# Kernel tuning notes

Hardware: AMD Instinct MI355X
Metric: run time of the kernel (lower is better)

The kernel has to match this reference:

```python
import jax, jax.numpy as jnp
import numpy as np

B, LAT, NF, IMG, N_CALLS = 8, 512, 64, 128, 4
N_LAYERS = int(np.ceil(np.log2(IMG) - np.log2(16))) + 1  # 4 resolutions: 16,32,64,128
CF = 3  # SinSobel perception factor: identity + sobel_x + sobel_y
FIN, FH, FOUT = NF * CF, NF, NF * 2  # gated => 2*n_filter out of dyna block
P_SIZES = [FH * FIN, FH, FOUT * FH, FOUT, FOUT * FIN, FOUT]
P_OFFS = np.cumsum([0] + P_SIZES)
P_TOT = int(P_OFFS[-1])

_g1 = np.exp(-0.5 * np.array([-1.0, 0.0, 1.0]) ** 2)
_gk = np.outer(_g1, _g1); _gk = _gk / _gk.sum()
GAUSS_K = jnp.asarray(_gk, jnp.float32)
SOBEL_X = jnp.asarray(np.array([[-1, 0, 1], [-2, 0, 2], [-1, 0, 1]], np.float32) / 8.0)
SOBEL_Y = SOBEL_X.T


def _dwconv3(x, k):
    # depthwise 3x3 conv, 'same' padding; x: [B,C,H,W], k: [3,3]
    C = x.shape[1]
    kern = jnp.broadcast_to(k[None, None], (C, 1, 3, 3)).astype(x.dtype)
    return jax.lax.conv_general_dilated(
        x, kern, (1, 1), ((1, 1), (1, 1)),
        dimension_numbers=('NCHW', 'OIHW', 'NCHW'), feature_group_count=C)


def sin_sobel(x):
    # perception: [x, sobel_x(x), sobel_y(x)] -> 3*C channels
    return jnp.concatenate([x, _dwconv3(x, SOBEL_X), _dwconv3(x, SOBEL_Y)], axis=1)


def inst_norm(x, eps=1e-5):
    m = x.mean((2, 3), keepdims=True)
    v = x.var((2, 3), keepdims=True)
    return (x - m) * jax.lax.rsqrt(v + eps)


def up2_blur(x, gk):
    b, c, h, w = x.shape
    x = jax.image.resize(x, (b, c, 2 * h, 2 * w), 'bilinear')  # align_corners=False
    return _dwconv3(x, gk)


def dyna_block(x, lat, hyper_w, hyper_b):
    # hypernetwork generates per-sample 1x1-conv residual block weights
    p = lat @ hyper_w + hyper_b  # [B, P_TOT]
    w1 = p[:, P_OFFS[0]:P_OFFS[1]].reshape(-1, FH, FIN)
    b1 = p[:, P_OFFS[1]:P_OFFS[2]]
    w2 = p[:, P_OFFS[2]:P_OFFS[3]].reshape(-1, FOUT, FH)
    b2 = p[:, P_OFFS[3]:P_OFFS[4]]
    ws = p[:, P_OFFS[4]:P_OFFS[5]].reshape(-1, FOUT, FIN)
    bs = p[:, P_OFFS[5]:P_OFFS[6]]
    h = jax.nn.relu(jnp.einsum('bihw,boi->bohw', x, w1) + b1[:, :, None, None])
    y = jnp.einsum('bihw,boi->bohw', h, w2) + b2[:, :, None, None]
    s = jnp.einsum('bihw,boi->bohw', x, ws) + bs[:, :, None, None]
    return s + y


def setup_inputs() -> dict:
    key = jax.random.key(0)
    ks = jax.random.split(key, 8)
    return dict(
        lat=jax.random.normal(ks[0], (B, LAT), jnp.float32),
        ca_noise=jax.random.normal(ks[1], (B, NF, 16, 16), jnp.float32),
        seed=jax.random.normal(ks[2], (1, NF, 1, 1), jnp.float32),  # spatially constant seed
        leak_factor=jnp.asarray(0.1, jnp.float32),
        hyper_w=jax.random.normal(ks[3], (LAT, P_TOT), jnp.float32) * 0.02,
        hyper_b=jnp.zeros((P_TOT,), jnp.float32),
        res1_w=jax.random.normal(ks[4], (NF, NF), jnp.float32) / np.sqrt(NF).astype(np.float32),
        res1_b=jnp.zeros((NF,), jnp.float32),
        res2_w=jax.random.normal(ks[5], (NF, NF), jnp.float32) / np.sqrt(NF).astype(np.float32),
        res2_b=jnp.zeros((NF,), jnp.float32),
        outc_w=jax.random.normal(ks[6], (3, NF), jnp.float32) / np.sqrt(NF).astype(np.float32),
        outc_b=jnp.zeros((3,), jnp.float32),
    )


def reference(lat, ca_noise, seed, leak_factor, hyper_w, hyper_b,
              res1_w, res1_b, res2_w, res2_b, outc_w, outc_b):
    # seed init branch: constant seed -> instance_norm -> 0, plus blurred ca_noise
    out = inst_norm(jnp.broadcast_to(seed, (B, NF, 16, 16)))
    out = out + _dwconv3(ca_noise, GAUSS_K)  # in_ds (resize 16->16 is identity)
    lf = jnp.clip(leak_factor, 0.001, 1000.0)
    for c in range(N_LAYERS * N_CALLS):
        z = sin_sobel(out)
        z = inst_norm(z)
        z = dyna_block(z, lat, hyper_w, hyper_b)
        z, g = jnp.split(z, 2, axis=1)  # gated
        z = z * jax.nn.sigmoid(g)
        out = out + lf * z
        if c < N_LAYERS * N_CALLS - 1 and c % N_CALLS == N_CALLS - 1:
            out = up2_blur(out, GAUSS_K)
    # out_conv: resize to IMG is identity here; 1x1 residual block + 1x1 conv
    h = jax.nn.relu(jnp.einsum('bihw,oi->bohw', out, res1_w) + res1_b[None, :, None, None])
    r = jnp.einsum('bihw,oi->bohw', h, res2_w) + res2_b[None, :, None, None]
    y = jnp.einsum('bihw,oi->bohw', out + r, outc_w) + outc_b[None, :, None, None]
    out_raw = y
    return jnp.clip(y, -1.0, 1.0), out_raw
```

## Files before the change

### kernel.cpp

```cpp
#include <hip/hip_runtime.h>
#include <math.h>

#define B 8
#define LATD 512
#define PT 45376
#define FIN 192
#define FH 64
#define OW1 0
#define OB1 12288
#define OW2 12352
#define OB2 20544
#define OWS 20672
#define OBS 45248
#define KC 16

__device__ __forceinline__ float gk_at(int ky, int kx){
  const float a = 0.60653065971263342f;
  const float inv = 1.0f / ((1.0f + 2.0f*a) * (1.0f + 2.0f*a));
  float wy = (ky==1) ? 1.0f : a;
  float wx = (kx==1) ? 1.0f : a;
  return wy * wx * inv;
}

__global__ void k_hyper(const float* __restrict__ lat, const float* __restrict__ hw,
                        const float* __restrict__ hb, float* __restrict__ p){
  __shared__ float slat[B*LATD];
  for (int idx = threadIdx.x; idx < B*LATD; idx += 256) slat[idx] = lat[idx];
  __syncthreads();
  int j = blockIdx.x*256 + threadIdx.x;
  if (j >= PT) return;
  float acc[B];
#pragma unroll
  for (int b=0;b<B;++b) acc[b]=0.f;
  for (int k=0;k<LATD;++k){
    float w = hw[(size_t)k*PT + j];
#pragma unroll
    for (int b=0;b<B;++b) acc[b] = fmaf(slat[b*LATD+k], w, acc[b]);
  }
  float bias = hb[j];
#pragma unroll
  for (int b=0;b<B;++b) p[(size_t)b*PT + j] = acc[b] + bias;
}

__global__ void k_init(const float* __restrict__ noise, float* __restrict__ out){
  int bc = blockIdx.x;
  int t = threadIdx.x;
  int y = t >> 4, x = t & 15;
  const float* src = noise + (size_t)bc*256;
  float acc = 0.f;
#pragma unroll
  for (int ky=0;ky<3;++ky){
    int yy = y+ky-1; if (yy < 0 || yy > 15) continue;
#pragma unroll
    for (int kx=0;kx<3;++kx){
      int xx = x+kx-1; if (xx < 0 || xx > 15) continue;
      acc = fmaf(gk_at(ky,kx), src[yy*16+xx], acc);
    }
  }
  out[(size_t)bc*256 + t] = acc;
}

__global__ void __launch_bounds__(256) k_sobstat(const float* __restrict__ out, float* __restrict__ sob,
                    float* __restrict__ stats, int H, int lgH, int HW){
  int flat = blockIdx.x; int b = flat & 7, c = flat >> 3;
  int t = threadIdx.x;
  const float* src = out + ((size_t)(b*64+c))*(size_t)HW;
  float* dxp = sob + ((size_t)(b*128 + c))*(size_t)HW;
  float* dyp = sob + ((size_t)(b*128 + 64 + c))*(size_t)HW;
  float s0=0.f,q0=0.f,sx=0.f,qx=0.f,sy=0.f,qy=0.f;
  for (int px = t*4; px < HW; px += 1024){
    int y = px >> lgH, x = px & (H-1);
    float rm[6], rc[6], rp[6];
    float4 v = *(const float4*)(src + px);
    rc[1]=v.x; rc[2]=v.y; rc[3]=v.z; rc[4]=v.w;
    rc[0] = (x>0)     ? src[px-1] : 0.f;
    rc[5] = (x+4 < H) ? src[px+4] : 0.f;
    s0 += v.x+v.y+v.z+v.w;
    q0 += v.x*v.x+v.y*v.y+v.z*v.z+v.w*v.w;
    if (y > 0){
      const float* r = src + px - H;
      float4 u = *(const float4*)r;
      rm[1]=u.x; rm[2]=u.y; rm[3]=u.z; rm[4]=u.w;
      rm[0] = (x>0)     ? r[-1] : 0.f;
      rm[5] = (x+4 < H) ? r[4]  : 0.f;
    } else { rm[0]=rm[1]=rm[2]=rm[3]=rm[4]=rm[5]=0.f; }
    if (y+1 < H){
      const float* r = src + px + H;
      float4 u = *(const float4*)r;
      rp[1]=u.x; rp[2]=u.y; rp[3]=u.z; rp[4]=u.w;
      rp[0] = (x>0)     ? r[-1] : 0.f;
      rp[5] = (x+4 < H) ? r[4]  : 0.f;
    } else { rp[0]=rp[1]=rp[2]=rp[3]=rp[4]=rp[5]=0.f; }
    float dxv[4], dyv[4];
#pragma unroll
    for (int j=0;j<4;++j){
      dxv[j] = ((rm[j+2]-rm[j]) + 2.f*(rc[j+2]-rc[j]) + (rp[j+2]-rp[j])) * 0.125f;
      dyv[j] = ((rp[j] + 2.f*rp[j+1] + rp[j+2]) - (rm[j] + 2.f*rm[j+1] + rm[j+2])) * 0.125f;
      sx += dxv[j]; qx = fmaf(dxv[j],dxv[j],qx);
      sy += dyv[j]; qy = fmaf(dyv[j],dyv[j],qy);
    }
    float4 o1; o1.x=dxv[0]; o1.y=dxv[1]; o1.z=dxv[2]; o1.w=dxv[3];
    float4 o2; o2.x=dyv[0]; o2.y=dyv[1]; o2.z=dyv[2]; o2.w=dyv[3];
    *(float4*)(dxp + px) = o1;
    *(float4*)(dyp + px) = o2;
  }
  float vals[6] = {s0,q0,sx,qx,sy,qy};
  __shared__ float rbuf[6][4];
  int lane = t & 63, wid = t >> 6;
#pragma unroll
  for (int i=0;i<6;++i){
    float v = vals[i];
#pragma unroll
    for (int off=32; off; off>>=1) v += __shfl_down(v, off, 64);
    if (lane==0) rbuf[i][wid] = v;
  }
  __syncthreads();
  if (t < 3){
    float s = rbuf[t*2][0]+rbuf[t*2][1]+rbuf[t*2][2]+rbuf[t*2][3];
    float q = rbuf[t*2+1][0]+rbuf[t*2+1][1]+rbuf[t*2+1][2]+rbuf[t*2+1][3];
    float inv = 1.0f/(float)HW;
    float m = s*inv;
    float var = fmaxf(q*inv - m*m, 0.f);
    float r = 1.0f/sqrtf(var + 1e-5f);
    int ch = b*192 + c + t*64;
    stats[ch*2]   = -m*r;
    stats[ch*2+1] = r;
  }
}

__device__ __forceinline__ float4 ldx(const float* __restrict__ out, const float* __restrict__ sob,
                                      const float* __restrict__ stats,
                                      int b, int i, int off, int HW){
  const float* src = (i < 64) ? out + ((size_t)(b*64+i))*(size_t)HW
                              : sob + ((size_t)(b*128+(i-64)))*(size_t)HW;
  float4 v = *(const float4*)(src + off);
  float c = stats[(b*192+i)*2], r = stats[(b*192+i)*2+1];
  v.x = fmaf(v.x, r, c); v.y = fmaf(v.y, r, c);
  v.z = fmaf(v.z, r, c); v.w = fmaf(v.w, r, c);
  return v;
}

template<int PPT>
__global__ void __launch_bounds__(256, 3) k_dyna(float* __restrict__ out, const float* __restrict__ sob,
                       const float* __restrict__ stats, const float* __restrict__ p,
                       const float* __restrict__ lfp, int HW){
  constexpr int G     = PPT/4;
  constexpr int TPXT  = 16*PPT;
  constexpr int XST   = TPXT + 4;
  constexpr int XHALF = KC*XST;
  constexpr int W1OFF = 2*XHALF;
  constexpr int W1HALF= KC*68;
  constexpr int WEND  = W1OFF + 2*W1HALF;
  constexpr int HSZ   = 64*XST;
  constexpr int ASZ   = (WEND > HSZ) ? WEND : HSZ;
  __shared__ float bufA[ASZ];
  __shared__ float bufB[2*KC*132];

  int flat = (int)(blockIdx.y*gridDim.x + blockIdx.x);
  int b   = flat & 7;
  int px0 = (flat >> 3) * TPXT;
  int tx = threadIdx.x, ty = threadIdx.y;
  int tid = ty*16 + tx;
  const float* pw = p + (size_t)b*PT;

  float az[4][PPT], ag[4][PPT], ah[4][PPT];
#pragma unroll
  for (int k=0;k<4;++k)
#pragma unroll
    for (int j=0;j<PPT;++j){ az[k][j]=0.f; ag[k][j]=0.f; ah[k][j]=0.f; }

  const int wo0 = tid>>2, wk = tid&3, wo1 = 64 + wo0;

  float4 vx[G], vz0, vz1, v10;

  auto loadX = [&](int ci){
#pragma unroll
    for (int g=0; g<G; ++g){
      int idx = g*256 + tid;
      vx[g] = ldx(out,sob,stats,b, ci*KC + idx/(4*PPT), px0 + (idx&(4*PPT-1))*4, HW);
    }
  };
  auto loadW1z = [&](int ci){
    vz0 = *(const float4*)(pw + OWS + wo0*FIN + ci*KC + wk*4);
    vz1 = *(const float4*)(pw + OWS + wo1*FIN + ci*KC + wk*4);
    v10 = *(const float4*)(pw + OW1 + wo0*FIN + ci*KC + wk*4);
  };
  auto loadW2 = [&](int ci){
    vz0 = *(const float4*)(pw + OW2 + wo0*FH + ci*KC + wk*4);
    vz1 = *(const float4*)(pw + OW2 + wo1*FH + ci*KC + wk*4);
  };
  auto writeX = [&](int bf){
#pragma unroll
    for (int g=0; g<G; ++g){
      int idx = g*256 + tid;
      *(float4*)(&bufA[bf*XHALF + (idx/(4*PPT))*XST + (idx&(4*PPT-1))*4]) = vx[g];
    }
  };
  auto writeWz = [&](int bf){
    float* WZ = &bufB[bf*(KC*132)];
    WZ[(wk*4+0)*132+wo0]=vz0.x; WZ[(wk*4+1)*132+wo0]=vz0.y; WZ[(wk*4+2)*132+wo0]=vz0.z; WZ[(wk*4+3)*132+wo0]=vz0.w;
    WZ[(wk*4+0)*132+wo1]=vz1.x; WZ[(wk*4+1)*132+wo1]=vz1.y; WZ[(wk*4+2)*132+wo1]=vz1.z; WZ[(wk*4+3)*132+wo1]=vz1.w;
  };
  auto writeW1 = [&](int bf){
    float* W1 = &bufA[W1OFF + bf*W1HALF];
    W1[(wk*4+0)*68+wo0]=v10.x; W1[(wk*4+1)*68+wo0]=v10.y; W1[(wk*4+2)*68+wo0]=v10.z; W1[(wk*4+3)*68+wo0]=v10.w;
  };
  auto computeA = [&](int bf){
#pragma unroll 4
    for (int kk=0; kk<KC; ++kk){
      float xv[PPT];
#pragma unroll
      for (int g=0; g<G; ++g){
        float4 xa = *(const float4*)(&bufA[bf*XHALF + kk*XST + (tx+g*16)*4]);
        xv[g*4+0]=xa.x; xv[g*4+1]=xa.y; xv[g*4+2]=xa.z; xv[g*4+3]=xa.w;
      }
      float4 wz4 = *(const float4*)(&bufB[bf*(KC*132) + kk*132 + ty*4]);
      float4 wg4 = *(const float4*)(&bufB[bf*(KC*132) + kk*132 + 64 + ty*4]);
      float4 w14 = *(const float4*)(&bufA[W1OFF + bf*W1HALF + kk*68 + ty*4]);
      float wzv[4]={wz4.x,wz4.y,wz4.z,wz4.w};
      float wgv[4]={wg4.x,wg4.y,wg4.z,wg4.w};
      float w1v[4]={w14.x,w14.y,w14.z,w14.w};
#pragma unroll
      for (int k=0;k<4;++k)
#pragma unroll
        for (int j=0;j<PPT;++j){
          az[k][j] = fmaf(wzv[k], xv[j], az[k][j]);
          ag[k][j] = fmaf(wgv[k], xv[j], ag[k][j]);
          ah[k][j] = fmaf(w1v[k], xv[j], ah[k][j]);
        }
    }
  };

  loadX(0); loadW1z(0);
  writeX(0); writeWz(0); writeW1(0);
  loadX(1); loadW1z(1);
  __syncthreads();
  for (int ci=0; ci<12; ++ci){
    int cur = ci & 1;
    if (ci < 11){ writeX(cur^1); writeWz(cur^1); writeW1(cur^1); }
    if (ci < 10){ loadX(ci+2); loadW1z(ci+2); }
    else if (ci == 10){ loadW2(0); }
    computeA(cur);
    __syncthreads();
  }

#pragma unroll
  for (int k=0;k<4;++k){
    float b1 = pw[OB1 + ty*4 + k];
#pragma unroll
    for (int h=0; h<G; ++h){
      float4 r;
      r.x = fmaxf(ah[k][h*4+0]+b1, 0.f);
      r.y = fmaxf(ah[k][h*4+1]+b1, 0.f);
      r.z = fmaxf(ah[k][h*4+2]+b1, 0.f);
      r.w = fmaxf(ah[k][h*4+3]+b1, 0.f);
      *(float4*)(&bufA[(ty*4+k)*XST + (tx+h*16)*4]) = r;
    }
  }
  writeWz(0);
  loadW2(1);
  __syncthreads();

  for (int ci=0; ci<4; ++ci){
    int cur = ci & 1;
    if (ci < 3) writeWz(cur^1);
    if (ci < 2) loadW2(ci+2);
#pragma unroll 4
    for (int kk=0; kk<KC; ++kk){
      float xv[PPT];
#pragma unroll
      for (int g=0; g<G; ++g){
        float4 xa = *(const float4*)(&bufA[(ci*KC+kk)*XST + (tx+g*16)*4]);
        xv[g*4+0]=xa.x; xv[g*4+1]=xa.y; xv[g*4+2]=xa.z; xv[g*4+3]=xa.w;
      }
      float4 wz4 = *(const float4*)(&bufB[cur*(KC*132) + kk*132 + ty*4]);
      float4 wg4 = *(const float4*)(&bufB[cur*(KC*132) + kk*132 + 64 + ty*4]);
      float wzv[4]={wz4.x,wz4.y,wz4.z,wz4.w};
      float wgv[4]={wg4.x,wg4.y,wg4.z,wg4.w};
#pragma unroll
      for (int k=0;k<4;++k)
#pragma unroll
        for (int j=0;j<PPT;++j){
          az[k][j] = fmaf(wzv[k], xv[j], az[k][j]);
          ag[k][j] = fmaf(wgv[k], xv[j], ag[k][j]);
        }
    }
    __syncthreads();
  }

  float lf = fminf(fmaxf(lfp[0], 0.001f), 1000.f);
#pragma unroll
  for (int k=0;k<4;++k){
    int o = ty*4 + k;
    float bz = pw[OB2 + o]      + pw[OBS + o];
    float bg = pw[OB2 + o + 64] + pw[OBS + o + 64];
    float* op = out + ((size_t)(b*64+o))*(size_t)HW + px0;
#pragma unroll
    for (int h=0; h<G; ++h){
      float4 ov = *(const float4*)(op + (tx + h*16)*4);
      float r[4];
#pragma unroll
      for (int j=0;j<4;++j){
        float z = az[k][h*4+j] + bz;
        float g = ag[k][h*4+j] + bg;
        r[j] = lf * z / (1.f + expf(-g));
      }
      ov.x += r[0]; ov.y += r[1]; ov.z += r[2]; ov.w += r[3];
      *(float4*)(op + (tx + h*16)*4) = ov;
    }
  }
}

__global__ void k_upsample(const float* __restrict__ src, float* __restrict__ dst, int H, int lgH){
  int Hn = 2*H;
  int HWn = Hn*Hn;
  int bc = blockIdx.y;
  int o4 = (blockIdx.x*256 + threadIdx.x)*4;
  const float* s = src + (size_t)bc*(size_t)(H*H);
  int oy = o4 >> (lgH+1), ox0 = o4 & (Hn-1);
  int m = ox0 >> 1;
  int xm1 = (m-1 < 0)   ? 0   : m-1;
  int xp1 = (m+1 > H-1) ? H-1 : m+1;
  int xp2 = (m+2 > H-1) ? H-1 : m+2;
  float u[3][6];
#pragma unroll
  for (int ky=0; ky<3; ++ky){
    int yy = oy + ky - 1;
    if (yy < 0 || yy >= Hn){
#pragma unroll
      for (int j=0;j<6;++j) u[ky][j] = 0.f;
      continue;
    }
    int iy = yy >> 1, ry = yy & 1;
    int y0 = ry ? iy : iy-1;
    int y1 = ry ? iy+1 : iy;
    float wy0 = ry ? 0.75f : 0.25f;
    float wy1 = 1.f - wy0;
    y0 = y0 < 0 ? 0 : y0;
    y1 = y1 > H-1 ? H-1 : y1;
    const float* r0 = s + y0*H;
    const float* r1 = s + y1*H;
    float sv0 = wy0*r0[xm1] + wy1*r1[xm1];
    float sv1 = wy0*r0[m]   + wy1*r1[m];
    float sv2 = wy0*r0[xp1] + wy1*r1[xp1];
    float sv3 = wy0*r0[xp2] + wy1*r1[xp2];
    u[ky][0] = 0.75f*sv0 + 0.25f*sv1;
    u[ky][1] = 0.25f*sv0 + 0.75f*sv1;
    u[ky][2] = 0.75f*sv1 + 0.25f*sv2;
    u[ky][3] = 0.25f*sv1 + 0.75f*sv2;
    u[ky][4] = 0.75f*sv2 + 0.25f*sv3;
    u[ky][5] = 0.25f*sv2 + 0.75f*sv3;
    if (ox0 == 0)       u[ky][0] = 0.f;
    if (ox0 + 4 == Hn)  u[ky][5] = 0.f;
  }
  float res[4];
#pragma unroll
  for (int jo=0; jo<4; ++jo){
    float a = 0.f;
#pragma unroll
    for (int ky=0; ky<3; ++ky){
      a = fmaf(gk_at(ky,0), u[ky][jo],   a);
      a = fmaf(gk_at(ky,1), u[ky][jo+1], a);
      a = fmaf(gk_at(ky,2), u[ky][jo+2], a);
    }
    res[jo] = a;
  }
  float4 o; o.x=res[0]; o.y=res[1]; o.z=res[2]; o.w=res[3];
  *(float4*)(dst + (size_t)bc*(size_t)HWn + o4) = o;
}

__global__ void __launch_bounds__(256) k_final(const float* __restrict__ t,
    const float* __restrict__ r1w, const float* __restrict__ r1b,
    const float* __restrict__ r2w, const float* __restrict__ r2b,
    const float* __restrict__ ocw, const float* __restrict__ ocb,
    float* __restrict__ dout, int HW){
  __shared__ float Ts[64][132];
  __shared__ float Hs[64][132];
  __shared__ float Wb[64][68];
  int b = blockIdx.y;
  int tx = threadIdx.x, ty = threadIdx.y;
  int tid = ty*16 + tx;
  int px0 = blockIdx.x*128;

#pragma unroll
  for (int it=0; it<8; ++it){
    int idx = it*256 + tid;
    int ch = idx>>5, c4 = idx&31;
    *(float4*)(&Ts[ch][c4*4]) = *(const float4*)(t + ((size_t)(b*64+ch))*(size_t)HW + px0 + c4*4);
  }
#pragma unroll
  for (int it=0; it<4; ++it){
    int idx = it*256 + tid;
    int o = idx>>4, k4 = idx&15;
    float4 w = *(const float4*)(r1w + o*64 + k4*4);
    Wb[k4*4+0][o]=w.x; Wb[k4*4+1][o]=w.y; Wb[k4*4+2][o]=w.z; Wb[k4*4+3][o]=w.w;
  }
  __syncthreads();

  float acc[4][8];
#pragma unroll
  for (int k=0;k<4;++k)
#pragma unroll
    for (int j=0;j<8;++j) acc[k][j]=0.f;
#pragma unroll 4
  for (int kk=0; kk<64; ++kk){
    float4 xa = *(const float4*)(&Ts[kk][tx*4]);
    float4 xb = *(const float4*)(&Ts[kk][(tx+16)*4]);
    float4 w4 = *(const float4*)(&Wb[kk][ty*4]);
    float xv[8]={xa.x,xa.y,xa.z,xa.w,xb.x,xb.y,xb.z,xb.w};
    float wv[4]={w4.x,w4.y,w4.z,w4.w};
#pragma unroll
    for (int k=0;k<4;++k)
#pragma unroll
      for (int j=0;j<8;++j) acc[k][j] = fmaf(wv[k], xv[j], acc[k][j]);
  }
  __syncthreads();

#pragma unroll
  for (int k=0;k<4;++k){
    float bs = r1b[ty*4+k];
#pragma unroll
    for (int h=0; h<2; ++h){
      float4 r;
      r.x = fmaxf(acc[k][h*4+0]+bs, 0.f);
      r.y = fmaxf(acc[k][h*4+1]+bs, 0.f);
      r.z = fmaxf(acc[k][h*4+2]+bs, 0.f);
      r.w = fmaxf(acc[k][h*4+3]+bs, 0.f);
      *(float4*)(&Hs[ty*4+k][(tx+h*16)*4]) = r;
    }
  }
#pragma unroll
  for (int it=0; it<4; ++it){
    int idx = it*256 + tid;
    int o = idx>>4, k4 = idx&15;
    float4 w = *(const float4*)(r2w + o*64 + k4*4);
    Wb[k4*4+0][o]=w.x; Wb[k4*4+1][o]=w.y; Wb[k4*4+2][o]=w.z; Wb[k4*4+3][o]=w.w;
  }
  __syncthreads();

#pragma unroll
  for (int k=0;k<4;++k)
#pragma unroll
    for (int j=0;j<8;++j) acc[k][j]=0.f;
#pragma unroll 4
  for (int kk=0; kk<64; ++kk){
    float4 xa = *(const float4*)(&Hs[kk][tx*4]);
    float4 xb = *(const float4*)(&Hs[kk][(tx+16)*4]);
    float4 w4 = *(const float4*)(&Wb[kk][ty*4]);
    float xv[8]={xa.x,xa.y,xa.z,xa.w,xb.x,xb.y,xb.z,xb.w};
    float wv[4]={w4.x,w4.y,w4.z,w4.w};
#pragma unroll
    for (int k=0;k<4;++k)
#pragma unroll
      for (int j=0;j<8;++j) acc[k][j] = fmaf(wv[k], xv[j], acc[k][j]);
  }
#pragma unroll
  for (int k=0;k<4;++k){
    int o = ty*4 + k;
    float bs = r2b[o];
#pragma unroll
    for (int h=0; h<2; ++h){
      float4 tv = *(const float4*)(&Ts[o][(tx+h*16)*4]);
      tv.x += acc[k][h*4+0]+bs; tv.y += acc[k][h*4+1]+bs;
      tv.z += acc[k][h*4+2]+bs; tv.w += acc[k][h*4+3]+bs;
      *(float4*)(&Ts[o][(tx+h*16)*4]) = tv;
    }
  }
  __syncthreads();
  if (tid < 192){
    int c = tid>>6, kk = tid&63;
    Wb[kk][c] = ocw[c*64+kk];
  }
  __syncthreads();

  if (tid < 128){
    float a0=0.f, a1=0.f, a2=0.f;
#pragma unroll 4
    for (int kk=0; kk<64; ++kk){
      float x = Ts[kk][tid];
      a0 = fmaf(x, Wb[kk][0], a0);
      a1 = fmaf(x, Wb[kk][1], a1);
      a2 = fmaf(x, Wb[kk][2], a2);
    }
    size_t rawoff = (size_t)B*3*(size_t)HW;
    float y[3] = {a0+ocb[0], a1+ocb[1], a2+ocb[2]};
    int px = px0 + tid;
#pragma unroll
    for (int c=0;c<3;++c){
      size_t base = ((size_t)(b*3+c))*(size_t)HW + px;
      dout[base] = fminf(fmaxf(y[c],-1.f),1.f);
      dout[rawoff + base] = y[c];
    }
  }
}

extern "C" void kernel_launch(void* const* d_in, const int* in_sizes, int n_in,
                              void* d_out, int out_size, void* d_ws, size_t ws_size,
                              hipStream_t stream) {
  const float* lat = (const float*)d_in[0];
  const float* ca  = (const float*)d_in[1];
  const float* lfp = (const float*)d_in[3];
  const float* hw  = (const float*)d_in[4];
  const float* hb  = (const float*)d_in[5];
  const float* r1w = (const float*)d_in[6];
  const float* r1b = (const float*)d_in[7];
  const float* r2w = (const float*)d_in[8];
  const float* r2b = (const float*)d_in[9];
  const float* ocw = (const float*)d_in[10];
  const float* ocb = (const float*)d_in[11];
  float* dout = (float*)d_out;

  float* ws   = (float*)d_ws;
  float* p    = ws;
  float* outA = p    + (size_t)B*PT;
  float* outB = outA + (size_t)B*64*16384;
  float* sob  = outB + (size_t)B*64*16384;
  float* stats= sob  + (size_t)B*128*16384;

  k_hyper<<<dim3((PT+255)/256), dim3(256), 0, stream>>>(lat, hw, hb, p);
  k_init<<<dim3(B*64), dim3(256), 0, stream>>>(ca, outA);

  float* cur = outA;
  float* oth = outB;
  int H = 16, lgH = 4;
  for (int c = 0; c < 16; ++c){
    int HW = H*H;
    k_sobstat<<<dim3(B*64), dim3(256), 0, stream>>>(cur, sob, stats, H, lgH, HW);
    if (H >= 128)
      k_dyna<8><<<dim3(HW/128, B), dim3(16,16), 0, stream>>>(cur, sob, stats, p, lfp, HW);
    else
      k_dyna<4><<<dim3(HW/64,  B), dim3(16,16), 0, stream>>>(cur, sob, stats, p, lfp, HW);
    if (c < 15 && (c & 3) == 3){
      k_upsample<<<dim3((HW*4)/1024, B*64), dim3(256), 0, stream>>>(cur, oth, H, lgH);
      float* tmp = cur; cur = oth; oth = tmp;
      H *= 2; lgH += 1;
    }
  }
  int HW = H*H;
  k_final<<<dim3(HW/128, B), dim3(16,16), 0, stream>>>(cur, r1w, r1b, r2w, r2b, ocw, ocb, dout, HW);
}
```

Measured before the change: 1.313 ms.

## Halve K-chunk and split hidden buffer to shrink LDS footprint in dyna kernel

Reduces the K chunk from 16 to 8 and narrows the padding strides. The hidden-activation staging area now holds only 32 channels, so the second GEMM stages the two halves of h in sequence with an extra barrier. Staging loads are also remapped to one float4 per thread. The goal is a smaller LDS footprint and fewer staging registers so more blocks fit per CU. The cost is twice as many pipeline iterations and barriers, plus possible bank conflicts from the new odd-ish strides.

Result: slower. 1.404 ms (+6.9%).

```diff
diff --git a/kernel.cpp b/kernel.cpp
--- a/kernel.cpp
+++ b/kernel.cpp
@@ -12,7 +12,7 @@
 #define OB2 20544
 #define OWS 20672
 #define OBS 45248
-#define KC 16
+#define KC 8
 
 __device__ __forceinline__ float gk_at(int ky, int kx){
   const float a = 0.60653065971263342f;
@@ -144,17 +144,21 @@
 __global__ void __launch_bounds__(256, 3) k_dyna(float* __restrict__ out, const float* __restrict__ sob,
                        const float* __restrict__ stats, const float* __restrict__ p,
                        const float* __restrict__ lfp, int HW){
-  constexpr int G     = PPT/4;
-  constexpr int TPXT  = 16*PPT;
-  constexpr int XST   = TPXT + 4;
-  constexpr int XHALF = KC*XST;
-  constexpr int W1OFF = 2*XHALF;
-  constexpr int W1HALF= KC*68;
-  constexpr int WEND  = W1OFF + 2*W1HALF;
-  constexpr int HSZ   = 64*XST;
-  constexpr int ASZ   = (WEND > HSZ) ? WEND : HSZ;
+  constexpr int G    = PPT/4;
+  constexpr int TPXT = 16*PPT;
+  constexpr int XST  = TPXT + 2;
+  constexpr int XH   = KC*XST;
+  constexpr int W1ST = 66;
+  constexpr int W1OFF= 2*XH;
+  constexpr int W1H  = KC*W1ST;
+  constexpr int AEND = W1OFF + 2*W1H;
+  constexpr int HSZ  = 32*XST;
+  constexpr int ASZ  = (AEND > HSZ) ? AEND : HSZ;
+  constexpr int WZST = 130;
+  constexpr int WZH  = KC*WZST;
+  constexpr int XTH  = KC*TPXT/4;
   __shared__ float bufA[ASZ];
-  __shared__ float bufB[2*KC*132];
+  __shared__ float bufB[2*WZH];
 
   int flat = (int)(blockIdx.y*gridDim.x + blockIdx.x);
   int b   = flat & 7;
@@ -169,41 +173,29 @@
 #pragma unroll
     for (int j=0;j<PPT;++j){ az[k][j]=0.f; ag[k][j]=0.f; ah[k][j]=0.f; }
 
-  const int wo0 = tid>>2, wk = tid&3, wo1 = 64 + wo0;
-
-  float4 vx[G], vz0, vz1, v10;
+  const int xch = tid / (TPXT/4), xc4 = tid % (TPXT/4);
+  const int wo  = tid >> 1,       wk  = tid & 1;
+
+  float4 vx, vz, v1;
 
   auto loadX = [&](int ci){
-#pragma unroll
-    for (int g=0; g<G; ++g){
-      int idx = g*256 + tid;
-      vx[g] = ldx(out,sob,stats,b, ci*KC + idx/(4*PPT), px0 + (idx&(4*PPT-1))*4, HW);
-    }
+    if (XTH==256 || tid<XTH) vx = ldx(out,sob,stats,b, ci*KC+xch, px0 + xc4*4, HW);
   };
-  auto loadW1z = [&](int ci){
-    vz0 = *(const float4*)(pw + OWS + wo0*FIN + ci*KC + wk*4);
-    vz1 = *(const float4*)(pw + OWS + wo1*FIN + ci*KC + wk*4);
-    v10 = *(const float4*)(pw + OW1 + wo0*FIN + ci*KC + wk*4);
-  };
-  auto loadW2 = [&](int ci){
-    vz0 = *(const float4*)(pw + OW2 + wo0*FH + ci*KC + wk*4);
-    vz1 = *(const float4*)(pw + OW2 + wo1*FH + ci*KC + wk*4);
-  };
+  auto loadWz = [&](int ci){ vz = *(const float4*)(pw + OWS + wo*FIN + ci*KC + wk*4); };
+  auto loadW1 = [&](int ci){ if (tid<128) v1 = *(const float4*)(pw + OW1 + wo*FIN + ci*KC + wk*4); };
+  auto loadW2 = [&](int ci){ vz = *(const float4*)(pw + OW2 + wo*FH + ci*KC + wk*4); };
   auto writeX = [&](int bf){
-#pragma unroll
-    for (int g=0; g<G; ++g){
-      int idx = g*256 + tid;
-      *(float4*)(&bufA[bf*XHALF + (idx/(4*PPT))*XST + (idx&(4*PPT-1))*4]) = vx[g];
-    }
+    if (XTH==256 || tid<XTH) *(float4*)(&bufA[bf*XH + xch*XST + xc4*4]) = vx;
   };
   auto writeWz = [&](int bf){
-    float* WZ = &bufB[bf*(KC*132)];
-    WZ[(wk*4+0)*132+wo0]=vz0.x; WZ[(wk*4+1)*132+wo0]=vz0.y; WZ[(wk*4+2)*132+wo0]=vz0.z; WZ[(wk*4+3)*132+wo0]=vz0.w;
-    WZ[(wk*4+0)*132+wo1]=vz1.x; WZ[(wk*4+1)*132+wo1]=vz1.y; WZ[(wk*4+2)*132+wo1]=vz1.z; WZ[(wk*4+3)*132+wo1]=vz1.w;
+    float* WZ = &bufB[bf*WZH + wo];
+    WZ[(wk*4+0)*WZST]=vz.x; WZ[(wk*4+1)*WZST]=vz.y; WZ[(wk*4+2)*WZST]=vz.z; WZ[(wk*4+3)*WZST]=vz.w;
   };
   auto writeW1 = [&](int bf){
-    float* W1 = &bufA[W1OFF + bf*W1HALF];
-    W1[(wk*4+0)*68+wo0]=v10.x; W1[(wk*4+1)*68+wo0]=v10.y; W1[(wk*4+2)*68+wo0]=v10.z; W1[(wk*4+3)*68+wo0]=v10.w;
+    if (tid<128){
+      float* W1 = &bufA[W1OFF + bf*W1H + wo];
+      W1[(wk*4+0)*W1ST]=v1.x; W1[(wk*4+1)*W1ST]=v1.y; W1[(wk*4+2)*W1ST]=v1.z; W1[(wk*4+3)*W1ST]=v1.w;
+    }
   };
   auto computeA = [&](int bf){
 #pragma unroll 4
@@ -211,12 +203,12 @@
       float xv[PPT];
 #pragma unroll
       for (int g=0; g<G; ++g){
-        float4 xa = *(const float4*)(&bufA[bf*XHALF + kk*XST + (tx+g*16)*4]);
+        float4 xa = *(const float4*)(&bufA[bf*XH + kk*XST + (tx+g*16)*4]);
         xv[g*4+0]=xa.x; xv[g*4+1]=xa.y; xv[g*4+2]=xa.z; xv[g*4+3]=xa.w;
       }
-      float4 wz4 = *(const float4*)(&bufB[bf*(KC*132) + kk*132 + ty*4]);
-      float4 wg4 = *(const float4*)(&bufB[bf*(KC*132) + kk*132 + 64 + ty*4]);
-      float4 w14 = *(const float4*)(&bufA[W1OFF + bf*W1HALF + kk*68 + ty*4]);
+      float4 wz4 = *(const float4*)(&bufB[bf*WZH + kk*WZST + ty*4]);
+      float4 wg4 = *(const float4*)(&bufB[bf*WZH + kk*WZST + 64 + ty*4]);
+      float4 w14 = *(const float4*)(&bufA[W1OFF + bf*W1H + kk*W1ST + ty*4]);
       float wzv[4]={wz4.x,wz4.y,wz4.z,wz4.w};
       float wgv[4]={wg4.x,wg4.y,wg4.z,wg4.w};
       float w1v[4]={w14.x,w14.y,w14.z,w14.w};
@@ -231,50 +223,52 @@
     }
   };
 
-  loadX(0); loadW1z(0);
+  loadX(0); loadWz(0); loadW1(0);
   writeX(0); writeWz(0); writeW1(0);
-  loadX(1); loadW1z(1);
-  __syncthreads();
-  for (int ci=0; ci<12; ++ci){
+  loadX(1); loadWz(1); loadW1(1);
+  __syncthreads();
+  for (int ci=0; ci<24; ++ci){
     int cur = ci & 1;
-    if (ci < 11){ writeX(cur^1); writeWz(cur^1); writeW1(cur^1); }
-    if (ci < 10){ loadX(ci+2); loadW1z(ci+2); }
-    else if (ci == 10){ loadW2(0); }
+    if (ci < 23){ writeX(cur^1); writeWz(cur^1); writeW1(cur^1); }
+    if (ci < 22){ loadX(ci+2); loadWz(ci+2); loadW1(ci+2); }
+    else if (ci == 22){ loadW2(0); }
     computeA(cur);
     __syncthreads();
   }
 
-#pragma unroll
-  for (int k=0;k<4;++k){
-    float b1 = pw[OB1 + ty*4 + k];
-#pragma unroll
-    for (int h=0; h<G; ++h){
-      float4 r;
-      r.x = fmaxf(ah[k][h*4+0]+b1, 0.f);
-      r.y = fmaxf(ah[k][h*4+1]+b1, 0.f);
-      r.z = fmaxf(ah[k][h*4+2]+b1, 0.f);
-      r.w = fmaxf(ah[k][h*4+3]+b1, 0.f);
-      *(float4*)(&bufA[(ty*4+k)*XST + (tx+h*16)*4]) = r;
+  if (ty < 8){
+#pragma unroll
+    for (int k=0;k<4;++k){
+      float b1 = pw[OB1 + ty*4 + k];
+#pragma unroll
+      for (int h=0; h<G; ++h){
+        float4 r;
+        r.x = fmaxf(ah[k][h*4+0]+b1, 0.f);
+        r.y = fmaxf(ah[k][h*4+1]+b1, 0.f);
+        r.z = fmaxf(ah[k][h*4+2]+b1, 0.f);
+        r.w = fmaxf(ah[k][h*4+3]+b1, 0.f);
+        *(float4*)(&bufA[(ty*4+k)*XST + (tx+h*16)*4]) = r;
+      }
     }
   }
   writeWz(0);
   loadW2(1);
   __syncthreads();
 
-  for (int ci=0; ci<4; ++ci){
+  for (int ci=0; ci<8; ++ci){
     int cur = ci & 1;
-    if (ci < 3) writeWz(cur^1);
-    if (ci < 2) loadW2(ci+2);
+    if (ci < 7) writeWz(cur^1);
+    if (ci < 6) loadW2(ci+2);
 #pragma unroll 4
     for (int kk=0; kk<KC; ++kk){
       float xv[PPT];
 #pragma unroll
       for (int g=0; g<G; ++g){
-        float4 xa = *(const float4*)(&bufA[(ci*KC+kk)*XST + (tx+g*16)*4]);
+        float4 xa = *(const float4*)(&bufA[((ci&3)*KC+kk)*XST + (tx+g*16)*4]);
         xv[g*4+0]=xa.x; xv[g*4+1]=xa.y; xv[g*4+2]=xa.z; xv[g*4+3]=xa.w;
       }
-      float4 wz4 = *(const float4*)(&bufB[cur*(KC*132) + kk*132 + ty*4]);
-      float4 wg4 = *(const float4*)(&bufB[cur*(KC*132) + kk*132 + 64 + ty*4]);
+      float4 wz4 = *(const float4*)(&bufB[cur*WZH + kk*WZST + ty*4]);
+      float4 wg4 = *(const float4*)(&bufB[cur*WZH + kk*WZST + 64 + ty*4]);
       float wzv[4]={wz4.x,wz4.y,wz4.z,wz4.w};
       float wgv[4]={wg4.x,wg4.y,wg4.z,wg4.w};
 #pragma unroll
@@ -286,6 +280,24 @@
         }
     }
     __syncthreads();
+    if (ci == 3){
+      if (ty >= 8){
+#pragma unroll
+        for (int k=0;k<4;++k){
+          float b1 = pw[OB1 + ty*4 + k];
+#pragma unroll
+          for (int h=0; h<G; ++h){
+            float4 r;
+            r.x = fmaxf(ah[k][h*4+0]+b1, 0.f);
+            r.y = fmaxf(ah[k][h*4+1]+b1, 0.f);
+            r.z = fmaxf(ah[k][h*4+2]+b1, 0.f);
+            r.w = fmaxf(ah[k][h*4+3]+b1, 0.f);
+            *(float4*)(&bufA[((ty-8)*4+k)*XST + (tx+h*16)*4]) = r;
+          }
+        }
+      }
+      __syncthreads();
+    }
   }
 
   float lf = fminf(fmaxf(lfp[0], 0.001f), 1000.f);
```

## Add 128-resolution dyna kernel with transposed weights read directly per wavefront

Applied to the files above, without the earlier changes.

Adds a repack kernel that transposes the per-sample hypernetwork weights into k-major layouts (combined skip+w1 and w2). A new 512-thread dyna kernel for the 128x128 layers keeps input tiles in shared memory, has each wave own 8 output channels, and reads weights as wave-uniform vector loads instead of staging them through shared memory. The second matmul streams relu hidden channels between waves through double-buffered shared memory. The aim is to cut shared-memory weight traffic and synchronisation in the dominant largest-resolution layers, at the cost of an extra repack launch, extra workspace, and a serialized hidden handoff.

Result: slower. 1.404 ms (+6.9%).

```diff
diff --git a/kernel.cpp b/kernel.cpp
--- a/kernel.cpp
+++ b/kernel.cpp
@@ -40,6 +40,24 @@
   float bias = hb[j];
 #pragma unroll
   for (int b=0;b<B;++b) p[(size_t)b*PT + j] = acc[b] + bias;
+}
+
+__global__ void k_repack(const float* __restrict__ p, float* __restrict__ WA, float* __restrict__ WC){
+  int idx = blockIdx.x*256 + threadIdx.x;
+  const int NA = 8*192*192;
+  const int NC = 8*64*128;
+  if (idx < NA){
+    int b = idx / (192*192); int r = idx - b*(192*192);
+    int k = r / 192, c = r - k*192;
+    const float* pb = p + (size_t)b*PT;
+    float v = (c < 128) ? pb[OWS + c*FIN + k] : pb[OW1 + (c-128)*FIN + k];
+    WA[idx] = v;
+  } else if (idx < NA + NC){
+    int i2 = idx - NA;
+    int b = i2 / (64*128); int r = i2 - b*(64*128);
+    int k = r / 128, c = r - k*128;
+    WC[i2] = p[(size_t)b*PT + OW2 + c*FH + k];
+  }
 }
 
 __global__ void k_init(const float* __restrict__ noise, float* __restrict__ out){
@@ -140,6 +158,134 @@
   return v;
 }
 
+__global__ void __launch_bounds__(512, 2) k_dyna256(float* __restrict__ out, const float* __restrict__ sob,
+                       const float* __restrict__ stats, const float* __restrict__ p,
+                       const float* __restrict__ WA, const float* __restrict__ WC,
+                       const float* __restrict__ lfp, int HW){
+  __shared__ float Xs[2][8][256];
+  int flat = blockIdx.x;
+  int b   = flat & 7;
+  int px0 = (flat >> 3) * 256;
+  int tx = threadIdx.x;
+  int w  = threadIdx.y;
+  int tid = w*64 + tx;
+  int o0 = __builtin_amdgcn_readfirstlane(w*8);
+  const float* pw = p  + (size_t)b*PT;
+  const float* wa = WA + (size_t)b*192*192;
+  const float* wc = WC + (size_t)b*64*128;
+
+  float az[8][4], ag[8][4], ah[8][4];
+#pragma unroll
+  for (int k=0;k<8;++k)
+#pragma unroll
+    for (int j=0;j<4;++j){ az[k][j]=0.f; ag[k][j]=0.f; ah[k][j]=0.f; }
+
+  const int sch = tid >> 6, sc4 = tid & 63;
+  float4 vx;
+  auto loadX  = [&](int ci){ vx = ldx(out,sob,stats,b, ci*8+sch, px0 + sc4*4, HW); };
+  auto writeX = [&](int bf){ *(float4*)(&Xs[bf][sch][sc4*4]) = vx; };
+
+  loadX(0); writeX(0); loadX(1);
+  __syncthreads();
+  for (int ci=0; ci<24; ++ci){
+    int cur = ci & 1;
+    if (ci < 23) writeX(cur^1);
+    if (ci < 22) loadX(ci+2);
+#pragma unroll
+    for (int kk=0; kk<8; ++kk){
+      const float* wr = wa + (size_t)(ci*8+kk)*192;
+      float4 x = *(const float4*)(&Xs[cur][kk][tx*4]);
+      float4 z0 = *(const float4*)(wr + o0);
+      float4 z1 = *(const float4*)(wr + o0 + 4);
+      float4 g0 = *(const float4*)(wr + 64 + o0);
+      float4 g1 = *(const float4*)(wr + 64 + o0 + 4);
+      float4 h0 = *(const float4*)(wr + 128 + o0);
+      float4 h1 = *(const float4*)(wr + 128 + o0 + 4);
+      float xv[4] = {x.x, x.y, x.z, x.w};
+      float wzv[8] = {z0.x,z0.y,z0.z,z0.w,z1.x,z1.y,z1.z,z1.w};
+      float wgv[8] = {g0.x,g0.y,g0.z,g0.w,g1.x,g1.y,g1.z,g1.w};
+      float whv[8] = {h0.x,h0.y,h0.z,h0.w,h1.x,h1.y,h1.z,h1.w};
+#pragma unroll
+      for (int k=0;k<8;++k)
+#pragma unroll
+        for (int j=0;j<4;++j){
+          az[k][j] = fmaf(wzv[k], xv[j], az[k][j]);
+          ag[k][j] = fmaf(wgv[k], xv[j], ag[k][j]);
+          ah[k][j] = fmaf(whv[k], xv[j], ah[k][j]);
+        }
+    }
+    __syncthreads();
+  }
+
+  if (w == 0){
+#pragma unroll
+    for (int k=0;k<8;++k){
+      float b1 = pw[OB1 + o0 + k];
+      float4 r;
+      r.x = fmaxf(ah[k][0]+b1, 0.f);
+      r.y = fmaxf(ah[k][1]+b1, 0.f);
+      r.z = fmaxf(ah[k][2]+b1, 0.f);
+      r.w = fmaxf(ah[k][3]+b1, 0.f);
+      *(float4*)(&Xs[0][k][tx*4]) = r;
+    }
+  }
+  __syncthreads();
+  for (int ci=0; ci<8; ++ci){
+    int cur = ci & 1;
+    if (ci < 7 && w == ci+1){
+#pragma unroll
+      for (int k=0;k<8;++k){
+        float b1 = pw[OB1 + o0 + k];
+        float4 r;
+        r.x = fmaxf(ah[k][0]+b1, 0.f);
+        r.y = fmaxf(ah[k][1]+b1, 0.f);
+        r.z = fmaxf(ah[k][2]+b1, 0.f);
+        r.w = fmaxf(ah[k][3]+b1, 0.f);
+        *(float4*)(&Xs[cur^1][k][tx*4]) = r;
+      }
+    }
+#pragma unroll
+    for (int kk=0; kk<8; ++kk){
+      const float* wr = wc + (size_t)(ci*8+kk)*128;
+      float4 x = *(const float4*)(&Xs[cur][kk][tx*4]);
+      float4 z0 = *(const float4*)(wr + o0);
+      float4 z1 = *(const float4*)(wr + o0 + 4);
+      float4 g0 = *(const float4*)(wr + 64 + o0);
+      float4 g1 = *(const float4*)(wr + 64 + o0 + 4);
+      float xv[4] = {x.x, x.y, x.z, x.w};
+      float wzv[8] = {z0.x,z0.y,z0.z,z0.w,z1.x,z1.y,z1.z,z1.w};
+      float wgv[8] = {g0.x,g0.y,g0.z,g0.w,g1.x,g1.y,g1.z,g1.w};
+#pragma unroll
+      for (int k=0;k<8;++k)
+#pragma unroll
+        for (int j=0;j<4;++j){
+          az[k][j] = fmaf(wzv[k], xv[j], az[k][j]);
+          ag[k][j] = fmaf(wgv[k], xv[j], ag[k][j]);
+        }
+    }
+    __syncthreads();
+  }
+
+  float lf = fminf(fmaxf(lfp[0], 0.001f), 1000.f);
+#pragma unroll
+  for (int k=0;k<8;++k){
+    int o = o0 + k;
+    float bz = pw[OB2 + o]      + pw[OBS + o];
+    float bg = pw[OB2 + o + 64] + pw[OBS + o + 64];
+    float* op = out + ((size_t)(b*64+o))*(size_t)HW + px0 + tx*4;
+    float4 ov = *(const float4*)op;
+    float r[4];
+#pragma unroll
+    for (int j=0;j<4;++j){
+      float z = az[k][j] + bz;
+      float g = ag[k][j] + bg;
+      r[j] = lf * z / (1.f + expf(-g));
+    }
+    ov.x += r[0]; ov.y += r[1]; ov.z += r[2]; ov.w += r[3];
+    *(float4*)op = ov;
+  }
+}
+
 template<int PPT>
 __global__ void __launch_bounds__(256, 3) k_dyna(float* __restrict__ out, const float* __restrict__ sob,
                        const float* __restrict__ stats, const float* __restrict__ p,
@@ -170,7 +316,6 @@
     for (int j=0;j<PPT;++j){ az[k][j]=0.f; ag[k][j]=0.f; ah[k][j]=0.f; }
 
   const int wo0 = tid>>2, wk = tid&3, wo1 = 64 + wo0;
-
   float4 vx[G], vz0, vz1, v10;
 
   auto loadX = [&](int ci){
@@ -516,8 +661,11 @@
   float* outB = outA + (size_t)B*64*16384;
   float* sob  = outB + (size_t)B*64*16384;
   float* stats= sob  + (size_t)B*128*16384;
+  float* WA   = stats+ (size_t)B*192*2;
+  float* WC   = WA   + (size_t)B*192*192;
 
   k_hyper<<<dim3((PT+255)/256), dim3(256), 0, stream>>>(lat, hw, hb, p);
+  k_repack<<<dim3((8*192*192 + 8*64*128 + 255)/256), dim3(256), 0, stream>>>(p, WA, WC);
   k_init<<<dim3(B*64), dim3(256), 0, stream>>>(ca, outA);
 
   float* cur = outA;
@@ -527,9 +675,9 @@
     int HW = H*H;
     k_sobstat<<<dim3(B*64), dim3(256), 0, stream>>>(cur, sob, stats, H, lgH, HW);
     if (H >= 128)
-      k_dyna<8><<<dim3(HW/128, B), dim3(16,16), 0, stream>>>(cur, sob, stats, p, lfp, HW);
+      k_dyna256<<<dim3((HW/256)*8), dim3(64,8), 0, stream>>>(cur, sob, stats, p, WA, WC, lfp, HW);
     else
-      k_dyna<4><<<dim3(HW/64,  B), dim3(16,16), 0, stream>>>(cur, sob, stats, p, lfp, HW);
+      k_dyna<4><<<dim3(HW/64, B), dim3(16,16), 0, stream>>>(cur, sob, stats, p, lfp, HW);
     if (c < 15 && (c & 3) == 3){
       k_upsample<<<dim3((HW*4)/1024, B*64), dim3(256), 0, stream>>>(cur, oth, H, lgH);
       float* tmp = cur; cur = oth; oth = tmp;
```
